# Optimization experiments

Measured on AMD Instinct MI355X. Metric: run time of the kernel, lower is better.

Reference implementation:

```python
import jax, jax.numpy as jnp
import numpy as np

B, T, D, W = 8, 16384, 2048, 4
GH = 128  # generator hidden = hidden_size // generator_reduction


def setup_inputs() -> dict:
    key = jax.random.key(0)
    ks = jax.random.split(key, 6)
    x = jax.random.normal(ks[0], (T, D), jnp.float32)
    generator_input = jax.random.normal(ks[1], (T, D), jnp.float32)
    w1 = jax.random.normal(ks[2], (D, GH), jnp.float32) * 0.02
    w2 = jax.random.normal(ks[3], (GH, D * W), jnp.float32) * 0.02
    b2 = jax.random.normal(ks[4], (D * W,), jnp.float32) * 0.02
    cache = jax.random.normal(ks[5], (B, D, W), jnp.float32)
    cu_seqlens = jnp.arange(B + 1, dtype=jnp.int32) * (T // B)
    seq_idx = jnp.repeat(jnp.arange(B, dtype=jnp.int32), T // B)
    cache_indices = jnp.arange(B, dtype=jnp.int32)
    has_initial_state = jnp.ones((B,), dtype=bool)
    return dict(x=x, generator_input=generator_input, w1=w1, w2=w2, b2=b2,
                cache=cache, cu_seqlens=cu_seqlens, seq_idx=seq_idx,
                cache_indices=cache_indices, has_initial_state=has_initial_state)


def reference(x, generator_input, w1, w2, b2, cache, cu_seqlens, seq_idx,
              cache_indices, has_initial_state):
    # --- per-token dynamic kernels: [T, D, W] ---
    h = jax.nn.silu(generator_input @ w1)          # [T, GH]
    kern = (h @ w2 + b2).reshape(T, D, W)          # [T, D, W]

    # --- causal dynamic depthwise conv over ragged sequences with cache ---
    t_idx = jnp.arange(T)
    pos = t_idx - cu_seqlens[seq_idx]              # position within own sequence
    ci = cache_indices[seq_idx]                    # [T] cache slot per token
    hi = has_initial_state[seq_idx]                # [T] bool

    out = jnp.zeros((T, D), x.dtype)
    for w in range(W):
        o = W - 1 - w                              # how far back this tap looks
        src = pos - o                              # in-sequence position of tap
        xg = x[jnp.clip(t_idx - o, 0, T - 1)]      # [T, D] gather from current tokens
        # cache slot W-1 holds the most recent previous token; src=-m -> slot W-m
        cg = cache[ci, :, jnp.clip(W + src, 0, W - 1)]  # [T, D]
        ctx = jnp.where((src >= 0)[:, None], xg,
                        jnp.where(hi[:, None], cg, jnp.zeros_like(xg)))
        out = out + kern[:, :, w] * ctx
    out = jax.nn.silu(out)

    # --- output_final_state: write last W-1 context tokens of each seq into cache ---
    starts = cu_seqlens[:-1]
    L = cu_seqlens[1:] - starts                    # [B] seq lengths
    kpos = jnp.arange(W - 1)                       # new slots 1..W-1
    rel = L[:, None] - (W - 1) + kpos[None, :]     # [B, W-1] in-seq position of token
    tok = starts[:, None] + rel                    # global token index
    xg = x[jnp.clip(tok, 0, T - 1)]                # [B, W-1, D]
    oldg = cache[cache_indices[:, None], :, jnp.clip(W + rel, 0, W - 1)]  # [B, W-1, D]
    existing = jnp.transpose(cache[cache_indices][:, :, 1:], (0, 2, 1))   # [B, W-1, D]
    hi_b = has_initial_state[:, None, None]
    new = jnp.where((rel >= 0)[:, :, None], xg, jnp.where(hi_b, oldg, existing))
    cache_new = cache.at[cache_indices, :, 1:].set(jnp.transpose(new, (0, 2, 1)))

    return out, cache_new
```

## Files before the change

kernel.cpp:

```cpp
#include <hip/hip_runtime.h>

#define T_DIM 16384
#define D_DIM 2048
#define GHD   128
#define W_DIM 4
#define B_DIM 8

typedef _Float16 f16x8 __attribute__((ext_vector_type(8)));
typedef float    f32x4 __attribute__((ext_vector_type(4)));

#define WS_W1F  0
#define WS_W2F  (512*1024)
#define WS_B2T  (WS_W2F + 2*1024*1024)
#define WS_HLIN (WS_B2T + 32*1024)

__global__ __launch_bounds__(256) void prep_kernel(
    const float* __restrict__ w1, const float* __restrict__ w2,
    const float* __restrict__ b2, _Float16* __restrict__ w1f,
    _Float16* __restrict__ w2f, float* __restrict__ b2t) {
  __shared__ float sm[4096];
  int bid = blockIdx.x, tid = threadIdx.x;
  int lane = tid & 63;
  int g = lane >> 4, c = lane & 15;

  if (bid < 512) {
    int df = bid >> 2, kk = bid & 3;
#pragma unroll
    for (int q = 0; q < 8; ++q) {
      int li = q * 256 + tid;
      int kl = li >> 6, nl = li & 63;
      sm[li] = w2[(size_t)(32 * kk + kl) * (D_DIM * W_DIM) + 64 * df + nl];
    }
    __syncthreads();
    int w = tid >> 6;
    f16x8 v;
#pragma unroll
    for (int i = 0; i < 8; ++i)
      v[i] = (_Float16)sm[(8 * g + i) * 64 + 4 * c + w];
    int fid = (w * 128 + df) * 4 + kk;
    *reinterpret_cast<f16x8*>(w2f + ((size_t)fid * 64 + lane) * 8) = v;
  } else if (bid < 576) {
    int kk = bid - 512;
#pragma unroll
    for (int q = 0; q < 16; ++q) {
      int li = q * 256 + tid;
      int kl = li >> 7, nl = li & 127;
      sm[li] = w1[(32 * kk + kl) * GHD + nl];
    }
    __syncthreads();
#pragma unroll
    for (int h = 0; h < 2; ++h) {
      int nf = (tid >> 6) * 2 + h;
      f16x8 v;
#pragma unroll
      for (int i = 0; i < 8; ++i)
        v[i] = (_Float16)sm[(8 * g + i) * GHD + 16 * nf + c];
      *reinterpret_cast<f16x8*>(w1f + ((size_t)(kk * 8 + nf) * 64 + lane) * 8) = v;
    }
  } else {
#pragma unroll
    for (int q = 0; q < 4; ++q) {
      int e = (bid - 576) * 1024 + q * 256 + tid;
      int w = e >> 11, d = e & 2047;
      b2t[w * D_DIM + d] = b2[d * 4 + w];
    }
  }
}

__global__ __launch_bounds__(256) void gemm1_kernel(
    const float* __restrict__ gen, const _Float16* __restrict__ w1f,
    _Float16* __restrict__ hlin) {
  int tid = threadIdx.x;
  int lane = tid & 63, wv = tid >> 6;
  int g = lane >> 4, c = lane & 15;
  int nf0 = 2 * wv;
  int row = blockIdx.x * 16 + c;
  const float* arow = gen + (size_t)row * D_DIM;

  f32x4 acc0 = {0.f, 0.f, 0.f, 0.f}, acc1 = {0.f, 0.f, 0.f, 0.f};

  for (int kk = 0; kk < 64; ++kk) {
    float4 a0 = *reinterpret_cast<const float4*>(arow + kk * 32 + 8 * g);
    float4 a1 = *reinterpret_cast<const float4*>(arow + kk * 32 + 8 * g + 4);
    f16x8 af;
    af[0] = (_Float16)a0.x; af[1] = (_Float16)a0.y;
    af[2] = (_Float16)a0.z; af[3] = (_Float16)a0.w;
    af[4] = (_Float16)a1.x; af[5] = (_Float16)a1.y;
    af[6] = (_Float16)a1.z; af[7] = (_Float16)a1.w;
    f16x8 b0 = *reinterpret_cast<const f16x8*>(
        w1f + ((size_t)(kk * 8 + nf0) * 64 + lane) * 8);
    f16x8 b1 = *reinterpret_cast<const f16x8*>(
        w1f + ((size_t)(kk * 8 + nf0 + 1) * 64 + lane) * 8);
    acc0 = __builtin_amdgcn_mfma_f32_16x16x32_f16(af, b0, acc0, 0, 0, 0);
    acc1 = __builtin_amdgcn_mfma_f32_16x16x32_f16(af, b1, acc1, 0, 0, 0);
  }
  int trow = blockIdx.x * 16 + 4 * g;
#pragma unroll
  for (int r = 0; r < 4; ++r) {
    float v0 = acc0[r];
    hlin[(size_t)(trow + r) * GHD + 16 * nf0 + c] =
        (_Float16)(v0 / (1.f + __expf(-v0)));
    float v1 = acc1[r];
    hlin[(size_t)(trow + r) * GHD + 16 * (nf0 + 1) + c] =
        (_Float16)(v1 / (1.f + __expf(-v1)));
  }
}

__global__ __launch_bounds__(256) void gemm2_int(
    const float* __restrict__ x, const _Float16* __restrict__ hlin,
    const _Float16* __restrict__ w2f, const float* __restrict__ b2t,
    float* __restrict__ out) {
  __shared__ float xs[4][35 * 36];
  int t_base = (blockIdx.x >> 5) * 64;
  if ((t_base & 2047) == 0) return;
  int tid = threadIdx.x;
  int lane = tid & 63, wv = tid >> 6;
  int wr = wv >> 1, wc = wv & 1;
  int g = lane >> 4, c = lane & 15;
  int d_base = (blockIdx.x & 31) * 64;
  float* myxs = xs[wv];

  {
    int colbase = d_base + 32 * wc;
    int r8 = lane >> 3, c4 = (lane & 7) * 4;
#pragma unroll
    for (int p = 0; p < 5; ++p) {
      int r = p * 8 + r8;
      if (r < 35) {
        int gr = t_base + 32 * wr - 3 + r;
        float4 v = *reinterpret_cast<const float4*>(
            x + (size_t)gr * D_DIM + colbase + c4);
        *reinterpret_cast<float4*>(&myxs[r * 36 + c4]) = v;
      }
    }
  }

  const _Float16* a0p = hlin + (size_t)(t_base + 32 * wr + c) * GHD + 8 * g;
  const _Float16* a1p = hlin + (size_t)(t_base + 32 * wr + 16 + c) * GHD + 8 * g;
  f16x8 A00 = *reinterpret_cast<const f16x8*>(a0p);
  f16x8 A01 = *reinterpret_cast<const f16x8*>(a0p + 32);
  f16x8 A02 = *reinterpret_cast<const f16x8*>(a0p + 64);
  f16x8 A03 = *reinterpret_cast<const f16x8*>(a0p + 96);
  f16x8 A10 = *reinterpret_cast<const f16x8*>(a1p);
  f16x8 A11 = *reinterpret_cast<const f16x8*>(a1p + 32);
  f16x8 A12 = *reinterpret_cast<const f16x8*>(a1p + 64);
  f16x8 A13 = *reinterpret_cast<const f16x8*>(a1p + 96);

  f32x4 oacc[2][2];
#pragma unroll
  for (int m = 0; m < 2; ++m) {
    oacc[m][0] = f32x4{0.f, 0.f, 0.f, 0.f};
    oacc[m][1] = f32x4{0.f, 0.f, 0.f, 0.f};
  }

  int df0 = (d_base >> 4) + 2 * wc;

#pragma unroll
  for (int w = 0; w < 4; ++w) {
    float bw0 = b2t[w * D_DIM + d_base + 32 * wc + c];
    float bw1 = b2t[w * D_DIM + d_base + 32 * wc + 16 + c];
    f32x4 acc[2][2];
#pragma unroll
    for (int m = 0; m < 2; ++m) {
      acc[m][0] = f32x4{0.f, 0.f, 0.f, 0.f};
      acc[m][1] = f32x4{0.f, 0.f, 0.f, 0.f};
    }
#pragma unroll
    for (int kk = 0; kk < 4; ++kk) {
      f16x8 B0 = *reinterpret_cast<const f16x8*>(
          w2f + ((size_t)((w * 128 + df0) * 4 + kk) * 64 + lane) * 8);
      f16x8 B1 = *reinterpret_cast<const f16x8*>(
          w2f + ((size_t)((w * 128 + df0 + 1) * 4 + kk) * 64 + lane) * 8);
      f16x8 Am0 = (kk == 0) ? A00 : (kk == 1) ? A01 : (kk == 2) ? A02 : A03;
      f16x8 Am1 = (kk == 0) ? A10 : (kk == 1) ? A11 : (kk == 2) ? A12 : A13;
      acc[0][0] = __builtin_amdgcn_mfma_f32_16x16x32_f16(Am0, B0, acc[0][0], 0, 0, 0);
      acc[0][1] = __builtin_amdgcn_mfma_f32_16x16x32_f16(Am0, B1, acc[0][1], 0, 0, 0);
      acc[1][0] = __builtin_amdgcn_mfma_f32_16x16x32_f16(Am1, B0, acc[1][0], 0, 0, 0);
      acc[1][1] = __builtin_amdgcn_mfma_f32_16x16x32_f16(Am1, B1, acc[1][1], 0, 0, 0);
    }
    int o = 3 - w;
#pragma unroll
    for (int m = 0; m < 2; ++m)
#pragma unroll
      for (int r = 0; r < 4; ++r) {
        int rl = 16 * m + 4 * g + r;
        float c0 = myxs[(rl + 3 - o) * 36 + c];
        float c1 = myxs[(rl + 3 - o) * 36 + 16 + c];
        oacc[m][0][r] += (acc[m][0][r] + bw0) * c0;
        oacc[m][1][r] += (acc[m][1][r] + bw1) * c1;
      }
  }

#pragma unroll
  for (int m = 0; m < 2; ++m)
#pragma unroll
    for (int r = 0; r < 4; ++r) {
      int t = t_base + 32 * wr + 16 * m + 4 * g + r;
#pragma unroll
      for (int n = 0; n < 2; ++n) {
        int col = d_base + 32 * wc + 16 * n + c;
        float v = oacc[m][n][r];
        out[(size_t)t * D_DIM + col] = v / (1.f + __expf(-v));
      }
    }
}

__global__ __launch_bounds__(256) void gemm2_bnd(
    const float* __restrict__ x, const _Float16* __restrict__ hlin,
    const _Float16* __restrict__ w2f, const float* __restrict__ b2t,
    const float* __restrict__ cache, const int* __restrict__ cu_seqlens,
    const int* __restrict__ seq_idx, const int* __restrict__ cache_indices,
    const unsigned char* __restrict__ hi_u8, const int* __restrict__ hi_i32,
    float* __restrict__ out) {
  __shared__ float xs[4][35 * 36];
  int tid = threadIdx.x;
  int lane = tid & 63, wv = tid >> 6;
  int wr = wv >> 1, wc = wv & 1;
  int g = lane >> 4, c = lane & 15;
  int t_base = (blockIdx.x >> 5) * 2048;
  int d_base = (blockIdx.x & 31) * 64;
  float* myxs = xs[wv];

  {
    int colbase = d_base + 32 * wc;
    int r8 = lane >> 3, c4 = (lane & 7) * 4;
#pragma unroll
    for (int p = 0; p < 5; ++p) {
      int r = p * 8 + r8;
      if (r < 35) {
        int gr = t_base + 32 * wr - 3 + r;
        gr = max(0, gr);
        float4 v = *reinterpret_cast<const float4*>(
            x + (size_t)gr * D_DIM + colbase + c4);
        *reinterpret_cast<float4*>(&myxs[r * 36 + c4]) = v;
      }
    }
  }

  float b2v[4][2];
#pragma unroll
  for (int w = 0; w < 4; ++w)
#pragma unroll
    for (int n = 0; n < 2; ++n)
      b2v[w][n] = b2t[w * D_DIM + d_base + 32 * wc + 16 * n + c];

  const _Float16* a0p = hlin + (size_t)(t_base + 32 * wr + c) * GHD + 8 * g;
  const _Float16* a1p = hlin + (size_t)(t_base + 32 * wr + 16 + c) * GHD + 8 * g;
  f16x8 A00 = *reinterpret_cast<const f16x8*>(a0p);
  f16x8 A01 = *reinterpret_cast<const f16x8*>(a0p + 32);
  f16x8 A02 = *reinterpret_cast<const f16x8*>(a0p + 64);
  f16x8 A03 = *reinterpret_cast<const f16x8*>(a0p + 96);
  f16x8 A10 = *reinterpret_cast<const f16x8*>(a1p);
  f16x8 A11 = *reinterpret_cast<const f16x8*>(a1p + 32);
  f16x8 A12 = *reinterpret_cast<const f16x8*>(a1p + 64);
  f16x8 A13 = *reinterpret_cast<const f16x8*>(a1p + 96);

  int meta[8];
#pragma unroll
  for (int m = 0; m < 2; ++m)
#pragma unroll
    for (int r = 0; r < 4; ++r) {
      int t = t_base + 32 * wr + 16 * m + 4 * g + r;
      int s = seq_idx[t];
      int pos = t - cu_seqlens[s];
      int ci = cache_indices[s];
      int hi = (hi_u8[s] != 0) | (hi_i32[s] != 0);
      meta[m * 4 + r] = pos | (ci << 16) | (hi << 24);
    }

  f32x4 oacc[2][2];
#pragma unroll
  for (int m = 0; m < 2; ++m) {
    oacc[m][0] = f32x4{0.f, 0.f, 0.f, 0.f};
    oacc[m][1] = f32x4{0.f, 0.f, 0.f, 0.f};
  }

  int df0 = (d_base >> 4) + 2 * wc;

#pragma unroll
  for (int w = 0; w < 4; ++w) {
    f32x4 acc[2][2];
#pragma unroll
    for (int m = 0; m < 2; ++m) {
      acc[m][0] = f32x4{0.f, 0.f, 0.f, 0.f};
      acc[m][1] = f32x4{0.f, 0.f, 0.f, 0.f};
    }
#pragma unroll
    for (int kk = 0; kk < 4; ++kk) {
      f16x8 B0 = *reinterpret_cast<const f16x8*>(
          w2f + ((size_t)((w * 128 + df0) * 4 + kk) * 64 + lane) * 8);
      f16x8 B1 = *reinterpret_cast<const f16x8*>(
          w2f + ((size_t)((w * 128 + df0 + 1) * 4 + kk) * 64 + lane) * 8);
      f16x8 Am0 = (kk == 0) ? A00 : (kk == 1) ? A01 : (kk == 2) ? A02 : A03;
      f16x8 Am1 = (kk == 0) ? A10 : (kk == 1) ? A11 : (kk == 2) ? A12 : A13;
      acc[0][0] = __builtin_amdgcn_mfma_f32_16x16x32_f16(Am0, B0, acc[0][0], 0, 0, 0);
      acc[0][1] = __builtin_amdgcn_mfma_f32_16x16x32_f16(Am0, B1, acc[0][1], 0, 0, 0);
      acc[1][0] = __builtin_amdgcn_mfma_f32_16x16x32_f16(Am1, B0, acc[1][0], 0, 0, 0);
      acc[1][1] = __builtin_amdgcn_mfma_f32_16x16x32_f16(Am1, B1, acc[1][1], 0, 0, 0);
    }
    int o = 3 - w;
#pragma unroll
    for (int m = 0; m < 2; ++m)
#pragma unroll
      for (int r = 0; r < 4; ++r) {
        int mt = meta[m * 4 + r];
        int pos = mt & 0xffff;
        int rl = 16 * m + 4 * g + r;
#pragma unroll
        for (int n = 0; n < 2; ++n) {
          int col = 32 * wc + 16 * n + c;
          float ctx;
          if (pos >= o) {
            ctx = myxs[(rl + 3 - o) * 36 + 16 * n + c];
          } else if ((mt >> 24) & 1) {
            int ci = (mt >> 16) & 0xff;
            ctx = cache[(size_t)ci * (D_DIM * W_DIM) +
                        (size_t)(d_base + col) * W_DIM + (4 + pos - o)];
          } else {
            ctx = 0.f;
          }
          oacc[m][n][r] += (acc[m][n][r] + b2v[w][n]) * ctx;
        }
      }
  }

#pragma unroll
  for (int m = 0; m < 2; ++m)
#pragma unroll
    for (int r = 0; r < 4; ++r) {
      int t = t_base + 32 * wr + 16 * m + 4 * g + r;
#pragma unroll
      for (int n = 0; n < 2; ++n) {
        int col = d_base + 32 * wc + 16 * n + c;
        float v = oacc[m][n][r];
        out[(size_t)t * D_DIM + col] = v / (1.f + __expf(-v));
      }
    }
}

__global__ __launch_bounds__(256) void cache_kernel(
    const float* __restrict__ x, const float* __restrict__ cache,
    const int* __restrict__ cu, const int* __restrict__ ci_arr,
    const unsigned char* __restrict__ hi_u8, const int* __restrict__ hi_i32,
    float* __restrict__ outc) {
  int idx = blockIdx.x * 256 + threadIdx.x;
  if (idx >= B_DIM * D_DIM * W_DIM) return;
  int b = idx >> 13, d = (idx >> 2) & 2047, j = idx & 3;
  float val = cache[idx];
  if (j >= 1) {
    for (int i = 0; i < B_DIM; ++i) {
      if (ci_arr[i] == b) {
        int L = cu[i + 1] - cu[i];
        int rel = L - (W_DIM - 1) + (j - 1);
        if (rel >= 0) {
          int tok = cu[i] + rel;
          tok = max(0, min(T_DIM - 1, tok));
          val = x[(size_t)tok * D_DIM + d];
        } else {
          bool hi = (hi_u8[i] != 0) | (hi_i32[i] != 0);
          int slot = 4 + rel;
          slot = max(0, min(3, slot));
          val = hi ? cache[b * (D_DIM * W_DIM) + d * 4 + slot]
                   : cache[b * (D_DIM * W_DIM) + d * 4 + j];
        }
      }
    }
  }
  outc[idx] = val;
}

extern "C" void kernel_launch(void* const* d_in, const int* in_sizes, int n_in,
                              void* d_out, int out_size, void* d_ws, size_t ws_size,
                              hipStream_t stream) {
  const float* x     = (const float*)d_in[0];
  const float* gen   = (const float*)d_in[1];
  const float* w1    = (const float*)d_in[2];
  const float* w2    = (const float*)d_in[3];
  const float* b2    = (const float*)d_in[4];
  const float* cache = (const float*)d_in[5];
  const int* cu      = (const int*)d_in[6];
  const int* seq     = (const int*)d_in[7];
  const int* cidx    = (const int*)d_in[8];
  const unsigned char* hi8 = (const unsigned char*)d_in[9];
  const int* hi32          = (const int*)d_in[9];
  float* out = (float*)d_out;

  char* ws = (char*)d_ws;
  _Float16* w1f  = (_Float16*)(ws + WS_W1F);
  _Float16* w2f  = (_Float16*)(ws + WS_W2F);
  float*    b2t  = (float*)(ws + WS_B2T);
  _Float16* hlin = (_Float16*)(ws + WS_HLIN);

  prep_kernel<<<dim3(584), dim3(256), 0, stream>>>(w1, w2, b2, w1f, w2f, b2t);
  gemm1_kernel<<<dim3(1024), dim3(256), 0, stream>>>(gen, w1f, hlin);
  gemm2_int<<<dim3(8192), dim3(256), 0, stream>>>(x, hlin, w2f, b2t, out);
  gemm2_bnd<<<dim3(256), dim3(256), 0, stream>>>(
      x, hlin, w2f, b2t, cache, cu, seq, cidx, hi8, hi32, out);
  cache_kernel<<<dim3(256), dim3(256), 0, stream>>>(
      x, cache, cu, cidx, hi8, hi32, out + (size_t)T_DIM * D_DIM);
}
```

Baseline: 197.3 us.

## Make gemm2_int persistent over 8 time tiles with register-prefetched x and hlin

Each gemm2_int block now loops over 8 consecutive 64-token tiles, launching 1024 blocks instead of 8192. The next tile's x rows and hlin A fragments are prefetched into registers while the current tile computes, and the LDS buffer is double-buffered. This hides global-load latency and amortises block launch cost. The trade-off is higher register pressure (launch bounds set to 3 blocks per SM), fewer blocks to balance load, and w2f B fragments reloaded on every tile.

```diff
diff --git a/kernel.cpp b/kernel.cpp
--- a/kernel.cpp
+++ b/kernel.cpp
@@ -5,6 +5,7 @@
 #define GHD   128
 #define W_DIM 4
 #define B_DIM 8
+#define NT    8
 
 typedef _Float16 f16x8 __attribute__((ext_vector_type(8)));
 typedef float    f32x4 __attribute__((ext_vector_type(4)));
@@ -106,103 +107,156 @@
   }
 }
 
-__global__ __launch_bounds__(256) void gemm2_int(
+__global__ __launch_bounds__(256, 3) void gemm2_int(
     const float* __restrict__ x, const _Float16* __restrict__ hlin,
     const _Float16* __restrict__ w2f, const float* __restrict__ b2t,
     float* __restrict__ out) {
-  __shared__ float xs[4][35 * 36];
-  int t_base = (blockIdx.x >> 5) * 64;
-  if ((t_base & 2047) == 0) return;
+  __shared__ float xs[2][4][35 * 36];
   int tid = threadIdx.x;
   int lane = tid & 63, wv = tid >> 6;
   int wr = wv >> 1, wc = wv & 1;
   int g = lane >> 4, c = lane & 15;
+  int t0 = (blockIdx.x >> 5) * (64 * NT);
   int d_base = (blockIdx.x & 31) * 64;
-  float* myxs = xs[wv];
+  int colbase = d_base + 32 * wc;
+  int r8 = lane >> 3, c4 = (lane & 7) * 4;
+  int df0 = (d_base >> 4) + 2 * wc;
+  const _Float16* wbase = w2f + (size_t)df0 * 4 * 64 * 8 + (size_t)lane * 8;
+
+  float4 xr[5], xrn[5];
+  f16x8 ar[4], arn[4];
 
   {
-    int colbase = d_base + 32 * wc;
-    int r8 = lane >> 3, c4 = (lane & 7) * 4;
 #pragma unroll
     for (int p = 0; p < 5; ++p) {
       int r = p * 8 + r8;
       if (r < 35) {
-        int gr = t_base + 32 * wr - 3 + r;
-        float4 v = *reinterpret_cast<const float4*>(
+        int gr = max(0, t0 + 32 * wr - 3 + r);
+        xr[p] = *reinterpret_cast<const float4*>(
             x + (size_t)gr * D_DIM + colbase + c4);
-        *reinterpret_cast<float4*>(&myxs[r * 36 + c4]) = v;
-      }
-    }
-  }
-
-  const _Float16* a0p = hlin + (size_t)(t_base + 32 * wr + c) * GHD + 8 * g;
-  const _Float16* a1p = hlin + (size_t)(t_base + 32 * wr + 16 + c) * GHD + 8 * g;
-  f16x8 A00 = *reinterpret_cast<const f16x8*>(a0p);
-  f16x8 A01 = *reinterpret_cast<const f16x8*>(a0p + 32);
-  f16x8 A02 = *reinterpret_cast<const f16x8*>(a0p + 64);
-  f16x8 A03 = *reinterpret_cast<const f16x8*>(a0p + 96);
-  f16x8 A10 = *reinterpret_cast<const f16x8*>(a1p);
-  f16x8 A11 = *reinterpret_cast<const f16x8*>(a1p + 32);
-  f16x8 A12 = *reinterpret_cast<const f16x8*>(a1p + 64);
-  f16x8 A13 = *reinterpret_cast<const f16x8*>(a1p + 96);
-
-  f32x4 oacc[2][2];
-#pragma unroll
-  for (int m = 0; m < 2; ++m) {
-    oacc[m][0] = f32x4{0.f, 0.f, 0.f, 0.f};
-    oacc[m][1] = f32x4{0.f, 0.f, 0.f, 0.f};
-  }
-
-  int df0 = (d_base >> 4) + 2 * wc;
-
-#pragma unroll
-  for (int w = 0; w < 4; ++w) {
-    float bw0 = b2t[w * D_DIM + d_base + 32 * wc + c];
-    float bw1 = b2t[w * D_DIM + d_base + 32 * wc + 16 + c];
-    f32x4 acc[2][2];
-#pragma unroll
-    for (int m = 0; m < 2; ++m) {
-      acc[m][0] = f32x4{0.f, 0.f, 0.f, 0.f};
-      acc[m][1] = f32x4{0.f, 0.f, 0.f, 0.f};
-    }
-#pragma unroll
-    for (int kk = 0; kk < 4; ++kk) {
-      f16x8 B0 = *reinterpret_cast<const f16x8*>(
-          w2f + ((size_t)((w * 128 + df0) * 4 + kk) * 64 + lane) * 8);
-      f16x8 B1 = *reinterpret_cast<const f16x8*>(
-          w2f + ((size_t)((w * 128 + df0 + 1) * 4 + kk) * 64 + lane) * 8);
-      f16x8 Am0 = (kk == 0) ? A00 : (kk == 1) ? A01 : (kk == 2) ? A02 : A03;
-      f16x8 Am1 = (kk == 0) ? A10 : (kk == 1) ? A11 : (kk == 2) ? A12 : A13;
-      acc[0][0] = __builtin_amdgcn_mfma_f32_16x16x32_f16(Am0, B0, acc[0][0], 0, 0, 0);
-      acc[0][1] = __builtin_amdgcn_mfma_f32_16x16x32_f16(Am0, B1, acc[0][1], 0, 0, 0);
-      acc[1][0] = __builtin_amdgcn_mfma_f32_16x16x32_f16(Am1, B0, acc[1][0], 0, 0, 0);
-      acc[1][1] = __builtin_amdgcn_mfma_f32_16x16x32_f16(Am1, B1, acc[1][1], 0, 0, 0);
-    }
-    int o = 3 - w;
-#pragma unroll
-    for (int m = 0; m < 2; ++m)
+      }
+    }
+    const _Float16* ap = hlin + (size_t)(t0 + 32 * wr + c) * GHD + 8 * g;
+#pragma unroll
+    for (int k = 0; k < 4; ++k)
+      ar[k] = *reinterpret_cast<const f16x8*>(ap + 32 * k);
+  }
+
+  for (int i = 0; i < NT; ++i) {
+    int t_base = t0 + i * 64;
+    float* myxs = xs[i & 1][wv];
+
+#pragma unroll
+    for (int p = 0; p < 5; ++p) {
+      int r = p * 8 + r8;
+      if (r < 35) *reinterpret_cast<float4*>(&myxs[r * 36 + c4]) = xr[p];
+    }
+
+    if (i + 1 < NT) {
+      int tn = t_base + 64;
+#pragma unroll
+      for (int p = 0; p < 5; ++p) {
+        int r = p * 8 + r8;
+        if (r < 35) {
+          int gr = tn + 32 * wr - 3 + r;
+          xrn[p] = *reinterpret_cast<const float4*>(
+              x + (size_t)gr * D_DIM + colbase + c4);
+        }
+      }
+      const _Float16* ap = hlin + (size_t)(tn + 32 * wr + c) * GHD + 8 * g;
+#pragma unroll
+      for (int k = 0; k < 4; ++k)
+        arn[k] = *reinterpret_cast<const f16x8*>(ap + 32 * k);
+    }
+
+    if ((t_base & 2047) != 0) {
+      f32x4 oacc[2];
+      oacc[0] = f32x4{0.f, 0.f, 0.f, 0.f};
+      oacc[1] = f32x4{0.f, 0.f, 0.f, 0.f};
+      f32x4 oacc2[2];
+      oacc2[0] = f32x4{0.f, 0.f, 0.f, 0.f};
+      oacc2[1] = f32x4{0.f, 0.f, 0.f, 0.f};
+
+#pragma unroll
+      for (int w = 0; w < 4; ++w) {
+        float bw0 = b2t[w * D_DIM + d_base + 32 * wc + c];
+        float bw1 = b2t[w * D_DIM + d_base + 32 * wc + 16 + c];
+        const _Float16* wp = wbase + (size_t)w * 128 * 4 * 64 * 8;
+        f16x8 B00 = *reinterpret_cast<const f16x8*>(wp + 0 * 512);
+        f16x8 B01 = *reinterpret_cast<const f16x8*>(wp + 1 * 512);
+        f16x8 B02 = *reinterpret_cast<const f16x8*>(wp + 2 * 512);
+        f16x8 B03 = *reinterpret_cast<const f16x8*>(wp + 3 * 512);
+        f16x8 B10 = *reinterpret_cast<const f16x8*>(wp + 4 * 512);
+        f16x8 B11 = *reinterpret_cast<const f16x8*>(wp + 5 * 512);
+        f16x8 B12 = *reinterpret_cast<const f16x8*>(wp + 6 * 512);
+        f16x8 B13 = *reinterpret_cast<const f16x8*>(wp + 7 * 512);
+
+        const _Float16* ap1 =
+            hlin + (size_t)(t_base + 32 * wr + 16 + c) * GHD + 8 * g;
+        f16x8 A10 = *reinterpret_cast<const f16x8*>(ap1);
+        f16x8 A11 = *reinterpret_cast<const f16x8*>(ap1 + 32);
+        f16x8 A12 = *reinterpret_cast<const f16x8*>(ap1 + 64);
+        f16x8 A13 = *reinterpret_cast<const f16x8*>(ap1 + 96);
+
+        f32x4 acc[2][2];
+        acc[0][0] = f32x4{0.f, 0.f, 0.f, 0.f};
+        acc[0][1] = f32x4{0.f, 0.f, 0.f, 0.f};
+        acc[1][0] = f32x4{0.f, 0.f, 0.f, 0.f};
+        acc[1][1] = f32x4{0.f, 0.f, 0.f, 0.f};
+
+        acc[0][0] = __builtin_amdgcn_mfma_f32_16x16x32_f16(ar[0], B00, acc[0][0], 0, 0, 0);
+        acc[1][0] = __builtin_amdgcn_mfma_f32_16x16x32_f16(A10,  B00, acc[1][0], 0, 0, 0);
+        acc[0][1] = __builtin_amdgcn_mfma_f32_16x16x32_f16(ar[0], B10, acc[0][1], 0, 0, 0);
+        acc[1][1] = __builtin_amdgcn_mfma_f32_16x16x32_f16(A10,  B10, acc[1][1], 0, 0, 0);
+        acc[0][0] = __builtin_amdgcn_mfma_f32_16x16x32_f16(ar[1], B01, acc[0][0], 0, 0, 0);
+        acc[1][0] = __builtin_amdgcn_mfma_f32_16x16x32_f16(A11,  B01, acc[1][0], 0, 0, 0);
+        acc[0][1] = __builtin_amdgcn_mfma_f32_16x16x32_f16(ar[1], B11, acc[0][1], 0, 0, 0);
+        acc[1][1] = __builtin_amdgcn_mfma_f32_16x16x32_f16(A11,  B11, acc[1][1], 0, 0, 0);
+        acc[0][0] = __builtin_amdgcn_mfma_f32_16x16x32_f16(ar[2], B02, acc[0][0], 0, 0, 0);
+        acc[1][0] = __builtin_amdgcn_mfma_f32_16x16x32_f16(A12,  B02, acc[1][0], 0, 0, 0);
+        acc[0][1] = __builtin_amdgcn_mfma_f32_16x16x32_f16(ar[2], B12, acc[0][1], 0, 0, 0);
+        acc[1][1] = __builtin_amdgcn_mfma_f32_16x16x32_f16(A12,  B12, acc[1][1], 0, 0, 0);
+        acc[0][0] = __builtin_amdgcn_mfma_f32_16x16x32_f16(ar[3], B03, acc[0][0], 0, 0, 0);
+        acc[1][0] = __builtin_amdgcn_mfma_f32_16x16x32_f16(A13,  B03, acc[1][0], 0, 0, 0);
+        acc[0][1] = __builtin_amdgcn_mfma_f32_16x16x32_f16(ar[3], B13, acc[0][1], 0, 0, 0);
+        acc[1][1] = __builtin_amdgcn_mfma_f32_16x16x32_f16(A13,  B13, acc[1][1], 0, 0, 0);
+
+        int o = 3 - w;
+#pragma unroll
+        for (int r = 0; r < 4; ++r) {
+          int rl0 = 4 * g + r;
+          int rl1 = 16 + 4 * g + r;
+          float c00 = myxs[(rl0 + 3 - o) * 36 + c];
+          float c01 = myxs[(rl0 + 3 - o) * 36 + 16 + c];
+          float c10 = myxs[(rl1 + 3 - o) * 36 + c];
+          float c11 = myxs[(rl1 + 3 - o) * 36 + 16 + c];
+          oacc[0][r]  += (acc[0][0][r] + bw0) * c00;
+          oacc[1][r]  += (acc[0][1][r] + bw1) * c01;
+          oacc2[0][r] += (acc[1][0][r] + bw0) * c10;
+          oacc2[1][r] += (acc[1][1][r] + bw1) * c11;
+        }
+      }
+
 #pragma unroll
       for (int r = 0; r < 4; ++r) {
-        int rl = 16 * m + 4 * g + r;
-        float c0 = myxs[(rl + 3 - o) * 36 + c];
-        float c1 = myxs[(rl + 3 - o) * 36 + 16 + c];
-        oacc[m][0][r] += (acc[m][0][r] + bw0) * c0;
-        oacc[m][1][r] += (acc[m][1][r] + bw1) * c1;
-      }
-  }
-
-#pragma unroll
-  for (int m = 0; m < 2; ++m)
-#pragma unroll
-    for (int r = 0; r < 4; ++r) {
-      int t = t_base + 32 * wr + 16 * m + 4 * g + r;
-#pragma unroll
-      for (int n = 0; n < 2; ++n) {
-        int col = d_base + 32 * wc + 16 * n + c;
-        float v = oacc[m][n][r];
-        out[(size_t)t * D_DIM + col] = v / (1.f + __expf(-v));
-      }
-    }
+        int tr0 = t_base + 32 * wr + 4 * g + r;
+        int tr1 = tr0 + 16;
+#pragma unroll
+        for (int n = 0; n < 2; ++n) {
+          int col = d_base + 32 * wc + 16 * n + c;
+          float v0 = oacc[n][r];
+          out[(size_t)tr0 * D_DIM + col] = v0 / (1.f + __expf(-v0));
+          float v1 = (n == 0) ? oacc2[0][r] : oacc2[1][r];
+          out[(size_t)tr1 * D_DIM + col] = v1 / (1.f + __expf(-v1));
+        }
+      }
+    }
+
+#pragma unroll
+    for (int p = 0; p < 5; ++p) xr[p] = xrn[p];
+#pragma unroll
+    for (int k = 0; k < 4; ++k) ar[k] = arn[k];
+  }
 }
 
 __global__ __launch_bounds__(256) void gemm2_bnd(
@@ -393,7 +447,7 @@
 
   prep_kernel<<<dim3(584), dim3(256), 0, stream>>>(w1, w2, b2, w1f, w2f, b2t);
   gemm1_kernel<<<dim3(1024), dim3(256), 0, stream>>>(gen, w1f, hlin);
-  gemm2_int<<<dim3(8192), dim3(256), 0, stream>>>(x, hlin, w2f, b2t, out);
+  gemm2_int<<<dim3(1024), dim3(256), 0, stream>>>(x, hlin, w2f, b2t, out);
   gemm2_bnd<<<dim3(256), dim3(256), 0, stream>>>(
       x, hlin, w2f, b2t, cache, cu, seq, cidx, hi8, hi32, out);
   cache_kernel<<<dim3(256), dim3(256), 0, stream>>>(
```

Measured after the change: 439.7 us. +122.9%, slower.
